# Kernel optimization log

Measured on AMD Instinct MI355X. Metric: run time of the kernel, lower is better.

## Reference

```python
import jax, jax.numpy as jnp
import numpy as np

N_NODES = 50000
N_EDGES = 1600000
IN_DIM = 256
OUT_DIM = 32
N_HEADS = 4
ALPHA = 0.2


def setup_inputs() -> dict:
    key = jax.random.key(0)
    k1, k2, k3, k4 = jax.random.split(key, 4)
    h = jax.random.normal(k1, (N_NODES, IN_DIM), dtype=jnp.float32)
    adj_indices = jax.random.randint(k2, (2, N_EDGES), 0, N_NODES, dtype=jnp.int32)
    # xavier_uniform with gain=1.414 (matching torch init scale)
    def xavier(k, shape, gain=1.414):
        fan_in, fan_out = shape[0], shape[1]
        lim = gain * np.sqrt(6.0 / (fan_in + fan_out))
        return jax.random.uniform(k, shape, jnp.float32, -lim, lim)
    W = xavier(k3, (IN_DIM, OUT_DIM * N_HEADS))
    a = xavier(k4, (2 * OUT_DIM, N_HEADS))
    return {"h": h, "adj_indices": adj_indices, "W": W, "a": a}


def reference(h, adj_indices, W, a):
    N = h.shape[0]
    # project: [N, H, D]
    h_prime = (h @ W).reshape(N, N_HEADS, OUT_DIM)
    src = adj_indices[0]
    dst = adj_indices[1]
    h_src = h_prime[src]  # [E, H, D]
    h_dst = h_prime[dst]  # [E, H, D]
    a_src = a[:OUT_DIM]   # [D, H]
    a_dst = a[OUT_DIM:]   # [D, H]
    # attention logits per edge, per head: [E, H]
    att = jnp.einsum('ehd,dh->eh', h_src, a_src) + jnp.einsum('ehd,dh->eh', h_dst, a_dst)
    att = jax.nn.leaky_relu(att, negative_slope=ALPHA)
    # scatter-softmax over destination nodes (stable)
    m = jax.ops.segment_max(att, dst, num_segments=N)          # [N, H]
    e = jnp.exp(att - m[dst])                                   # [E, H]
    s = jax.ops.segment_sum(e, dst, num_segments=N)             # [N, H]
    att_norm = e / s[dst]                                       # [E, H]
    # weighted scatter-add aggregation: [N, H, D]
    agg = jax.ops.segment_sum(att_norm[:, :, None] * h_src, dst, num_segments=N)
    out = agg.reshape(N, N_HEADS * OUT_DIM)
    # dropout=0.0 (eval / identity)
    return out
```

## Files before the change

### kernel.cpp

```cpp
#include <hip/hip_runtime.h>

#define N_NODES 50000
#define N_EDGES 1600000
#define IN_DIM  256
#define OUT_D   128
#define NEG_SLOPE 0.2f
#define NBIN 256
#define BINW 196
#define CAP  8192
#define NFINE 8
#define FBINW 25
#define LCAP 1152
#define GEMM_BLOCKS 391
#define BINA_BLOCKS 196

typedef unsigned short ushort_t;
typedef short bf16x8 __attribute__((ext_vector_type(8)));
typedef float f32x4 __attribute__((ext_vector_type(4)));

__device__ __forceinline__ ushort_t f2bf(float f) {
    unsigned u = __float_as_uint(f);
    u = (u + 0x7FFF + ((u >> 16) & 1)) >> 16;
    return (ushort_t)u;
}

__global__ __launch_bounds__(256) void wprep_kernel(const float* __restrict__ W,
                                                    ushort_t* __restrict__ wt) {
    int i0 = (blockIdx.x * 256 + threadIdx.x) * 4;
    f32x4 v = *(const f32x4*)(W + i0);
    int k = i0 >> 7;
    int n0 = i0 & 127;
#pragma unroll
    for (int j = 0; j < 4; ++j)
        wt[((n0 + j) << 8) + k] = f2bf(v[j]);
}

__global__ __launch_bounds__(256, 4) void gemmbin_kernel(
        const float* __restrict__ h, const ushort_t* __restrict__ wt,
        const float* __restrict__ a,
        const int* __restrict__ src, const int* __restrict__ dst,
        ushort_t* __restrict__ hp, float* __restrict__ asrc,
        float* __restrict__ adst,
        int* __restrict__ tail, unsigned* __restrict__ binbuf) {
    int t = threadIdx.x;
    if (blockIdx.x < GEMM_BLOCKS) {
        int wave = t >> 6, lane = t & 63;
        int l15 = lane & 15, quad = lane >> 4;
        int rowbase = blockIdx.x * 128 + wave * 16;

        f32x4 acc[2][8] = {};
#pragma unroll
        for (int ks = 0; ks < 8; ++ks) {
            bf16x8 af[2];
#pragma unroll
            for (int rt = 0; rt < 2; ++rt) {
                int arow = rowbase + rt * 64 + l15;
                if (arow >= N_NODES) arow = N_NODES - 1;
                const float* ap = h + (size_t)arow * IN_DIM + quad * 8 + ks * 32;
                f32x4 lo = *(const f32x4*)ap;
                f32x4 hi = *(const f32x4*)(ap + 4);
#pragma unroll
                for (int j = 0; j < 4; ++j) {
                    af[rt][j]     = (short)f2bf(lo[j]);
                    af[rt][4 + j] = (short)f2bf(hi[j]);
                }
            }
#pragma unroll
            for (int tn = 0; tn < 8; ++tn) {
                int n = tn * 16 + l15;
                bf16x8 bfr = *(const bf16x8*)(wt + (n << 8) + ks * 32 + quad * 8);
                acc[0][tn] = __builtin_amdgcn_mfma_f32_16x16x32_bf16(af[0], bfr, acc[0][tn], 0, 0, 0);
                acc[1][tn] = __builtin_amdgcn_mfma_f32_16x16x32_bf16(af[1], bfr, acc[1][tn], 0, 0, 0);
            }
        }

        float aS[8], aD[8];
#pragma unroll
        for (int tn = 0; tn < 8; ++tn) {
            int col = tn * 16 + l15;
            int dd = col & 31, hh = col >> 5;
            aS[tn] = a[dd * 4 + hh];
            aD[tn] = a[(32 + dd) * 4 + hh];
        }

#pragma unroll
        for (int rt = 0; rt < 2; ++rt)
#pragma unroll
            for (int r = 0; r < 4; ++r) {
                int row = rowbase + rt * 64 + quad * 4 + r;
                float pS[4] = {0.f, 0.f, 0.f, 0.f}, pD[4] = {0.f, 0.f, 0.f, 0.f};
#pragma unroll
                for (int tn = 0; tn < 8; ++tn) {
                    float v = acc[rt][tn][r];
                    pS[tn >> 1] += v * aS[tn];
                    pD[tn >> 1] += v * aD[tn];
                }
#pragma unroll
                for (int o = 1; o < 16; o <<= 1) {
#pragma unroll
                    for (int hh = 0; hh < 4; ++hh) {
                        pS[hh] += __shfl_xor(pS[hh], o, 16);
                        pD[hh] += __shfl_xor(pD[hh], o, 16);
                    }
                }
                if (row < N_NODES) {
                    if (l15 == 0) { f32x4 v = {pS[0], pS[1], pS[2], pS[3]}; *(f32x4*)(asrc + row * 4) = v; }
                    if (l15 == 1) { f32x4 v = {pD[0], pD[1], pD[2], pD[3]}; *(f32x4*)(adst + row * 4) = v; }
                }
            }

#pragma unroll
        for (int rt = 0; rt < 2; ++rt)
#pragma unroll
            for (int tn = 0; tn < 8; ++tn) {
                int col = tn * 16 + l15;
#pragma unroll
                for (int r = 0; r < 4; ++r) {
                    int row = rowbase + rt * 64 + quad * 4 + r;
                    if (row < N_NODES) hp[(size_t)row * OUT_D + col] = f2bf(acc[rt][tn][r]);
                }
            }
    } else {
        __shared__ unsigned stage[8192];
        __shared__ int cnt[256], lcnt[256], lbase[256], gbase[256], sc[256];
        int bid = blockIdx.x - GEMM_BLOCKS;
        cnt[t] = 0; lcnt[t] = 0;
        __syncthreads();

        int blockbase = bid * 8192;
        int n = min(8192, N_EDGES - blockbase);
        int e0 = blockbase + t * 32;
        int d[32], s[32];
#pragma unroll
        for (int q = 0; q < 8; ++q) {
            if (t * 32 + q * 4 + 4 <= n) {
                int4 dv = *(const int4*)(dst + e0 + q * 4);
                int4 sv = *(const int4*)(src + e0 + q * 4);
                d[q*4+0]=dv.x; d[q*4+1]=dv.y; d[q*4+2]=dv.z; d[q*4+3]=dv.w;
                s[q*4+0]=sv.x; s[q*4+1]=sv.y; s[q*4+2]=sv.z; s[q*4+3]=sv.w;
            } else {
#pragma unroll
                for (int r = 0; r < 4; ++r) {
                    int g = t * 32 + q * 4 + r;
                    d[q*4+r] = (g < n) ? dst[e0 + q*4 + r] : -1;
                    s[q*4+r] = (g < n) ? src[e0 + q*4 + r] : 0;
                }
            }
        }
#pragma unroll
        for (int j = 0; j < 32; ++j)
            if (d[j] >= 0) atomicAdd(&cnt[(unsigned)d[j] / BINW], 1);
        __syncthreads();
        gbase[t] = atomicAdd(&tail[t], cnt[t]);
        sc[t] = cnt[t]; __syncthreads();
#pragma unroll
        for (int off = 1; off < 256; off <<= 1) {
            int v = (t >= off) ? sc[t - off] : 0;
            __syncthreads();
            sc[t] += v;
            __syncthreads();
        }
        lbase[t] = sc[t] - cnt[t];
        __syncthreads();
#pragma unroll
        for (int j = 0; j < 32; ++j) {
            if (d[j] >= 0) {
                unsigned p = (unsigned)d[j] / BINW;
                unsigned ldst = (unsigned)d[j] - p * BINW;
                int pos = lbase[p] + atomicAdd(&lcnt[p], 1);
                stage[pos] = (unsigned)s[j] | (ldst << 16) | (p << 24);
            }
        }
        __syncthreads();
        for (int i = t; i < n; i += 256) {
            unsigned v = stage[i];
            unsigned p = v >> 24;
            int pos = gbase[p] + (i - lbase[p]);
            if (pos < CAP) binbuf[(size_t)p * CAP + pos] = v & 0xFFFFFFu;
        }
    }
}

__global__ __launch_bounds__(256) void binB_kernel(const int* __restrict__ tail,
                                                   unsigned* __restrict__ binbuf,
                                                   int* __restrict__ fbase,
                                                   int* __restrict__ fcnt) {
    int b = blockIdx.x, t = threadIdx.x;
    __shared__ unsigned stg[CAP];
    __shared__ int wtot[4][NFINE];
    __shared__ int jbase[NFINE];
    int wave = t >> 6, lane = t & 63;
    int count = min(tail[b], CAP);
    unsigned* buf = binbuf + (size_t)b * CAP;

    int chunk = (count + 255) >> 8;
    int lo = min(t * chunk, count), hi = min(lo + chunk, count);

    int c[NFINE] = {0, 0, 0, 0, 0, 0, 0, 0};
    for (int i = lo; i < hi; ++i) {
        int j = (int)(buf[i] >> 16) / FBINW;
#pragma unroll
        for (int jj = 0; jj < NFINE; ++jj) c[jj] += (j == jj) ? 1 : 0;
    }
    int myb[NFINE];
#pragma unroll
    for (int jj = 0; jj < NFINE; ++jj) {
        int v = c[jj];
#pragma unroll
        for (int off = 1; off < 64; off <<= 1) {
            int u = __shfl_up(v, off, 64);
            if (lane >= off) v += u;
        }
        myb[jj] = v - c[jj];
        if (lane == 63) wtot[wave][jj] = v;
    }
    __syncthreads();
    if (t == 0) {
        int runj[NFINE];
#pragma unroll
        for (int jj = 0; jj < NFINE; ++jj) {
            int r = 0;
#pragma unroll
            for (int w = 0; w < 4; ++w) { int x = wtot[w][jj]; wtot[w][jj] = r; r += x; }
            runj[jj] = r;
        }
        int r = 0;
#pragma unroll
        for (int jj = 0; jj < NFINE; ++jj) {
            jbase[jj] = r;
            fbase[b * NFINE + jj] = r;
            fcnt [b * NFINE + jj] = runj[jj];
            r += runj[jj];
        }
    }
    __syncthreads();
    int pos[NFINE];
#pragma unroll
    for (int jj = 0; jj < NFINE; ++jj) pos[jj] = jbase[jj] + wtot[wave][jj] + myb[jj];
    for (int i = lo; i < hi; ++i) {
        unsigned v = buf[i];
        int ldst = (int)(v >> 16);
        int j = ldst / FBINW;
        int p = 0;
#pragma unroll
        for (int jj = 0; jj < NFINE; ++jj) p = (j == jj) ? pos[jj] : p;
        stg[p] = (v & 0xFFFFu) | ((unsigned)(ldst - j * FBINW) << 16);
#pragma unroll
        for (int jj = 0; jj < NFINE; ++jj) pos[jj] += (j == jj) ? 1 : 0;
    }
    __syncthreads();
    for (int i = t; i < count; i += 256) buf[i] = stg[i];
}

__global__ __launch_bounds__(256) void aggB_kernel(const unsigned* __restrict__ binbuf,
                                                   const int* __restrict__ fbase,
                                                   const int* __restrict__ fcnt,
                                                   const float* __restrict__ asrc,
                                                   const float* __restrict__ adst,
                                                   const ushort_t* __restrict__ hp,
                                                   float* __restrict__ out) {
    int bid = blockIdx.x;
    int b = bid >> 3, fj = bid & 7;
    __shared__ ushort_t lcsr[LCAP];
    __shared__ int cnt[32], sc[32], excl[32], lcur[32];
    __shared__ int   s_i[4][64];
    __shared__ f32x4 s_p[4][64];
    int t = threadIdx.x;
    int count = min(fcnt[bid], LCAP);
    const unsigned* buf = binbuf + (size_t)b * CAP + fbase[bid];
    int dbase = b * BINW + fj * FBINW;
    int nd = min(FBINW, BINW - fj * FBINW);

    if (t < 32) cnt[t] = 0;
    __syncthreads();
    for (int i = t; i < count; i += 256)
        atomicAdd(&cnt[(buf[i] >> 16) & 31], 1);
    __syncthreads();
    if (t < 64) {
        int v = (t < 32) ? cnt[t] : 0;
#pragma unroll
        for (int off = 1; off < 32; off <<= 1) {
            int u = __shfl_up(v, off, 64);
            if (t >= off) v += u;
        }
        if (t < 32) { sc[t] = v; excl[t] = v - cnt[t]; lcur[t] = v - cnt[t]; }
    }
    __syncthreads();
    for (int i = t; i < count; i += 256) {
        unsigned v = buf[i];
        int ld = (v >> 16) & 31;
        int pos = atomicAdd(&lcur[ld], 1);
        lcsr[pos] = (ushort_t)(v & 0xFFFF);
    }
    __syncthreads();

    int wave = t >> 6, lane = t & 63;
    int l15 = lane & 15, grp = lane >> 4;
    int hd = l15 >> 2;

    for (int ld = wave; ld < nd; ld += 4) {
        int d = dbase + ld;
        if (d >= N_NODES) continue;
        int s0 = excl[ld], s1 = sc[ld];
        f32x4 ad = *(const f32x4*)(adst + d * 4);
        float sum[4] = {0.f, 0.f, 0.f, 0.f};
        f32x4 accA = {0.f, 0.f, 0.f, 0.f}, accB = {0.f, 0.f, 0.f, 0.f};

        for (int base = s0; base < s1; base += 64) {
            int n = min(64, s1 - base);
            int e = base + lane;
            bool ok = e < s1;
            int s = ok ? (int)lcsr[e] : 0;
            f32x4 p4 = {0.f, 0.f, 0.f, 0.f};
            if (ok) {
                f32x4 as = *(const f32x4*)(asrc + s * 4);
#pragma unroll
                for (int hh = 0; hh < 4; ++hh) {
                    float v = as[hh] + ad[hh];
                    v = v > 0.f ? v : NEG_SLOPE * v;
                    v = fminf(v, 80.f);
                    float p = __expf(v);
                    p4[hh] = p;
                    sum[hh] += p;
                }
            }
            s_i[wave][lane] = s;
            s_p[wave][lane] = p4;
            __builtin_amdgcn_wave_barrier();
            int iters = (n + 3) >> 2;
#pragma unroll 2
            for (int it = 0; it < iters; ++it) {
                int ei = it * 4 + grp;
                int se = s_i[wave][ei];
                float w = s_p[wave][ei][hd];
                const char* rp = (const char*)hp + ((size_t)se << 8) + l15 * 16;
                uint4 u = *(const uint4*)rp;
                accA[0] += w * __uint_as_float(u.x << 16);
                accA[1] += w * __uint_as_float(u.x & 0xFFFF0000u);
                accA[2] += w * __uint_as_float(u.y << 16);
                accA[3] += w * __uint_as_float(u.y & 0xFFFF0000u);
                accB[0] += w * __uint_as_float(u.z << 16);
                accB[1] += w * __uint_as_float(u.z & 0xFFFF0000u);
                accB[2] += w * __uint_as_float(u.w << 16);
                accB[3] += w * __uint_as_float(u.w & 0xFFFF0000u);
            }
            __builtin_amdgcn_wave_barrier();
        }
#pragma unroll
        for (int o = 16; o < 64; o <<= 1) {
#pragma unroll
            for (int q = 0; q < 4; ++q) {
                accA[q] += __shfl_xor(accA[q], o, 64);
                accB[q] += __shfl_xor(accB[q], o, 64);
            }
        }
#pragma unroll
        for (int o = 1; o < 64; o <<= 1) {
#pragma unroll
            for (int hh = 0; hh < 4; ++hh) sum[hh] += __shfl_xor(sum[hh], o, 64);
        }
        if (grp == 0) {
            float den = sum[hd];
            float inv = (den > 0.f) ? 1.f / den : 0.f;
            f32x4 r0, r1;
#pragma unroll
            for (int q = 0; q < 4; ++q) { r0[q] = accA[q] * inv; r1[q] = accB[q] * inv; }
            float* op = out + (size_t)d * OUT_D + l15 * 8;
            *(f32x4*)op = r0;
            *(f32x4*)(op + 4) = r1;
        }
    }
}

extern "C" void kernel_launch(void* const* d_in, const int* in_sizes, int n_in,
                              void* d_out, int out_size, void* d_ws, size_t ws_size,
                              hipStream_t stream) {
    const float* h   = (const float*)d_in[0];
    const int*   adj = (const int*)d_in[1];
    const float* W   = (const float*)d_in[2];
    const float* a   = (const float*)d_in[3];
    float*       out = (float*)d_out;

    const int* src = adj;
    const int* dst = adj + N_EDGES;

    char* ws = (char*)d_ws;
    size_t o = 0;
    auto alloc = [&](size_t bytes) -> void* {
        void* p = ws + o;
        o = (o + bytes + 255) & ~(size_t)255;
        return p;
    };
    ushort_t* hp     = (ushort_t*)alloc((size_t)N_NODES * OUT_D * 2);
    ushort_t* wt     = (ushort_t*)alloc((size_t)32768 * 2);
    float*    asrc   = (float*)alloc((size_t)N_NODES * 4 * 4);
    float*    adstp  = (float*)alloc((size_t)N_NODES * 4 * 4);
    int*      tail   = (int*)alloc((size_t)NBIN * 4);
    unsigned* binbuf = (unsigned*)alloc((size_t)NBIN * CAP * 4);
    int*      fbase  = (int*)alloc((size_t)NBIN * NFINE * 4);
    int*      fcnt   = (int*)alloc((size_t)NBIN * NFINE * 4);

    hipMemsetAsync(tail, 0, (size_t)NBIN * 4, stream);

    wprep_kernel<<<32, 256, 0, stream>>>(W, wt);
    gemmbin_kernel<<<GEMM_BLOCKS + BINA_BLOCKS, 256, 0, stream>>>(
        h, wt, a, src, dst, hp, asrc, adstp, tail, binbuf);
    binB_kernel<<<NBIN, 256, 0, stream>>>(tail, binbuf, fbase, fcnt);
    aggB_kernel<<<NBIN * NFINE, 256, 0, stream>>>(binbuf, fbase, fcnt, asrc, adstp, hp, out);
}
```

Measured before the change: 203.8 us.

## Prefetch next node's edge data in aggregation, simplify fine-binning with LDS atomics

The aggregation kernel now software-pipelines across destination nodes: while it processes the first 64-edge chunk of the current node, it loads the next node's CSR range, adst and asrc values. The intent is to hide gather latency between nodes. The fine-binning kernel swaps per-thread contiguous chunks, wave scans and register position arrays for shared-memory atomic histograms and cursors, and uses a multiply-shift in place of division. Launch bounds ask for 8 blocks per SM. The atomic scatter makes element order within each fine bin nondeterministic, and the prefetch adds register pressure.

New measurement: 208.7 us. 2.4% more time.

```diff
diff --git a/kernel.cpp b/kernel.cpp
--- a/kernel.cpp
+++ b/kernel.cpp
@@ -187,78 +187,47 @@
                                                    int* __restrict__ fcnt) {
     int b = blockIdx.x, t = threadIdx.x;
     __shared__ unsigned stg[CAP];
-    __shared__ int wtot[4][NFINE];
-    __shared__ int jbase[NFINE];
-    int wave = t >> 6, lane = t & 63;
+    __shared__ int hist[NFINE], jcur[NFINE];
     int count = min(tail[b], CAP);
     unsigned* buf = binbuf + (size_t)b * CAP;
 
-    int chunk = (count + 255) >> 8;
-    int lo = min(t * chunk, count), hi = min(lo + chunk, count);
-
-    int c[NFINE] = {0, 0, 0, 0, 0, 0, 0, 0};
-    for (int i = lo; i < hi; ++i) {
-        int j = (int)(buf[i] >> 16) / FBINW;
-#pragma unroll
-        for (int jj = 0; jj < NFINE; ++jj) c[jj] += (j == jj) ? 1 : 0;
-    }
-    int myb[NFINE];
-#pragma unroll
-    for (int jj = 0; jj < NFINE; ++jj) {
-        int v = c[jj];
-#pragma unroll
-        for (int off = 1; off < 64; off <<= 1) {
-            int u = __shfl_up(v, off, 64);
-            if (lane >= off) v += u;
-        }
-        myb[jj] = v - c[jj];
-        if (lane == 63) wtot[wave][jj] = v;
+    if (t < NFINE) hist[t] = 0;
+    __syncthreads();
+    for (int i = t; i < count; i += 256) {
+        int ldst = (int)(buf[i] >> 16);
+        int j = (ldst * 5243) >> 17;
+        atomicAdd(&hist[j], 1);
     }
     __syncthreads();
     if (t == 0) {
-        int runj[NFINE];
+        int r = 0;
 #pragma unroll
         for (int jj = 0; jj < NFINE; ++jj) {
-            int r = 0;
-#pragma unroll
-            for (int w = 0; w < 4; ++w) { int x = wtot[w][jj]; wtot[w][jj] = r; r += x; }
-            runj[jj] = r;
-        }
-        int r = 0;
-#pragma unroll
-        for (int jj = 0; jj < NFINE; ++jj) {
-            jbase[jj] = r;
+            jcur[jj] = r;
             fbase[b * NFINE + jj] = r;
-            fcnt [b * NFINE + jj] = runj[jj];
-            r += runj[jj];
-        }
-    }
-    __syncthreads();
-    int pos[NFINE];
-#pragma unroll
-    for (int jj = 0; jj < NFINE; ++jj) pos[jj] = jbase[jj] + wtot[wave][jj] + myb[jj];
-    for (int i = lo; i < hi; ++i) {
+            fcnt [b * NFINE + jj] = hist[jj];
+            r += hist[jj];
+        }
+    }
+    __syncthreads();
+    for (int i = t; i < count; i += 256) {
         unsigned v = buf[i];
         int ldst = (int)(v >> 16);
-        int j = ldst / FBINW;
-        int p = 0;
-#pragma unroll
-        for (int jj = 0; jj < NFINE; ++jj) p = (j == jj) ? pos[jj] : p;
+        int j = (ldst * 5243) >> 17;
+        int p = atomicAdd(&jcur[j], 1);
         stg[p] = (v & 0xFFFFu) | ((unsigned)(ldst - j * FBINW) << 16);
-#pragma unroll
-        for (int jj = 0; jj < NFINE; ++jj) pos[jj] += (j == jj) ? 1 : 0;
     }
     __syncthreads();
     for (int i = t; i < count; i += 256) buf[i] = stg[i];
 }
 
-__global__ __launch_bounds__(256) void aggB_kernel(const unsigned* __restrict__ binbuf,
-                                                   const int* __restrict__ fbase,
-                                                   const int* __restrict__ fcnt,
-                                                   const float* __restrict__ asrc,
-                                                   const float* __restrict__ adst,
-                                                   const ushort_t* __restrict__ hp,
-                                                   float* __restrict__ out) {
+__global__ __launch_bounds__(256, 8) void aggB_kernel(const unsigned* __restrict__ binbuf,
+                                                      const int* __restrict__ fbase,
+                                                      const int* __restrict__ fcnt,
+                                                      const float* __restrict__ asrc,
+                                                      const float* __restrict__ adst,
+                                                      const ushort_t* __restrict__ hp,
+                                                      float* __restrict__ out) {
     int bid = blockIdx.x;
     int b = bid >> 3, fj = bid & 7;
     __shared__ ushort_t lcsr[LCAP];
@@ -298,15 +267,78 @@
     int l15 = lane & 15, grp = lane >> 4;
     int hd = l15 >> 2;
 
+    int d_c = 0, s0_c = 0, s1_c = 0, s_c = 0;
+    f32x4 ad_c = (f32x4){0.f, 0.f, 0.f, 0.f}, as_c = (f32x4){0.f, 0.f, 0.f, 0.f};
+    if (wave < nd) {
+        d_c = dbase + wave;
+        s0_c = excl[wave]; s1_c = sc[wave];
+        if (d_c < N_NODES) ad_c = *(const f32x4*)(adst + d_c * 4);
+        int e = s0_c + lane;
+        s_c = (e < s1_c) ? (int)lcsr[e] : 0;
+        as_c = *(const f32x4*)(asrc + s_c * 4);
+    }
+
     for (int ld = wave; ld < nd; ld += 4) {
-        int d = dbase + ld;
-        if (d >= N_NODES) continue;
-        int s0 = excl[ld], s1 = sc[ld];
-        f32x4 ad = *(const f32x4*)(adst + d * 4);
+        int d = d_c, s0 = s0_c, s1 = s1_c, scur = s_c;
+        f32x4 ad = ad_c, as0 = as_c;
+
         float sum[4] = {0.f, 0.f, 0.f, 0.f};
         f32x4 accA = {0.f, 0.f, 0.f, 0.f}, accB = {0.f, 0.f, 0.f, 0.f};
 
-        for (int base = s0; base < s1; base += 64) {
+        {
+            bool ok = (s0 + lane) < s1;
+            f32x4 p4 = {0.f, 0.f, 0.f, 0.f};
+            if (ok) {
+#pragma unroll
+                for (int hh = 0; hh < 4; ++hh) {
+                    float v = as0[hh] + ad[hh];
+                    v = v > 0.f ? v : NEG_SLOPE * v;
+                    v = fminf(v, 80.f);
+                    float p = __expf(v);
+                    p4[hh] = p;
+                    sum[hh] += p;
+                }
+            }
+            s_i[wave][lane] = scur;
+            s_p[wave][lane] = p4;
+        }
+        __builtin_amdgcn_wave_barrier();
+
+        int ldn = ld + 4;
+        d_c = 0; s0_c = 0; s1_c = 0; s_c = 0;
+        ad_c = (f32x4){0.f, 0.f, 0.f, 0.f}; as_c = (f32x4){0.f, 0.f, 0.f, 0.f};
+        if (ldn < nd) {
+            d_c = dbase + ldn;
+            s0_c = excl[ldn]; s1_c = sc[ldn];
+            if (d_c < N_NODES) ad_c = *(const f32x4*)(adst + d_c * 4);
+            int e = s0_c + lane;
+            s_c = (e < s1_c) ? (int)lcsr[e] : 0;
+            as_c = *(const f32x4*)(asrc + s_c * 4);
+        }
+
+        int n1 = min(64, s1 - s0);
+        if (n1 > 0) {
+            int iters = (n1 + 3) >> 2;
+#pragma unroll 2
+            for (int it = 0; it < iters; ++it) {
+                int ei = it * 4 + grp;
+                int se = s_i[wave][ei];
+                float w = s_p[wave][ei][hd];
+                const char* rp = (const char*)hp + ((size_t)se << 8) + l15 * 16;
+                uint4 u = *(const uint4*)rp;
+                accA[0] += w * __uint_as_float(u.x << 16);
+                accA[1] += w * __uint_as_float(u.x & 0xFFFF0000u);
+                accA[2] += w * __uint_as_float(u.y << 16);
+                accA[3] += w * __uint_as_float(u.y & 0xFFFF0000u);
+                accB[0] += w * __uint_as_float(u.z << 16);
+                accB[1] += w * __uint_as_float(u.z & 0xFFFF0000u);
+                accB[2] += w * __uint_as_float(u.w << 16);
+                accB[3] += w * __uint_as_float(u.w & 0xFFFF0000u);
+            }
+        }
+        __builtin_amdgcn_wave_barrier();
+
+        for (int base = s0 + 64; base < s1; base += 64) {
             int n = min(64, s1 - base);
             int e = base + lane;
             bool ok = e < s1;
@@ -346,6 +378,7 @@
             }
             __builtin_amdgcn_wave_barrier();
         }
+
 #pragma unroll
         for (int o = 16; o < 64; o <<= 1) {
 #pragma unroll
@@ -359,7 +392,7 @@
 #pragma unroll
             for (int hh = 0; hh < 4; ++hh) sum[hh] += __shfl_xor(sum[hh], o, 64);
         }
-        if (grp == 0) {
+        if (grp == 0 && d < N_NODES) {
             float den = sum[hd];
             float inv = (den > 0.f) ? 1.f / den : 0.f;
             f32x4 r0, r1;
```
